# Kernel tuning notes

Hardware: AMD Instinct MI355X
Metric: run time of the kernel (lower is better)

## Reference

```python
import jax, jax.numpy as jnp
import numpy as np

B, LQ, LK, DK, DV = 32, 128, 4096, 256, 256


def setup_inputs() -> dict:
    key = jax.random.key(0)
    k1, k2, k3, k4, k5 = jax.random.split(key, 5)
    return {
        "query": jax.random.normal(k1, (B, LQ, DK), dtype=jnp.float32),
        "query_lengths": jax.random.randint(k2, (B,), 1, LQ, dtype=jnp.int32),
        "keys": jax.random.normal(k3, (B, LK, DK), dtype=jnp.float32),
        "values": jax.random.normal(k4, (B, LK, DV), dtype=jnp.float32),
        "mask": jax.random.randint(k5, (B, LK), 0, 2, dtype=jnp.int32),  # 1 = masked out
    }


def reference(query, query_lengths, keys, values, mask):
    # zero query positions beyond each example's length (torch: mask_query masked_fill 0)
    q_valid = jnp.arange(query.shape[1])[None, :] < query_lengths[:, None]  # [B, Lq]
    query = jnp.where(q_valid[:, :, None], query, 0.0)
    # zero masked key/value timesteps (torch mask: 1 -> masked)
    kv_valid = (mask == 0)[:, :, None]  # [B, Lk, 1]
    keys = jnp.where(kv_valid, keys, 0.0)
    values = jnp.where(kv_valid, values, 0.0)
    # attention scores [B, Lq, Lk]
    weights = jnp.einsum("bqd,bkd->bqk", query, keys)
    # exact-zero scores (masked rows/cols) -> -inf, matching torch weights==0.0 fill
    weights = jnp.where(weights == 0.0, -jnp.inf, weights)
    weights = jax.nn.softmax(weights, axis=-1)
    # rows that were all -inf produce NaN -> cleaned to 0
    weights = jnp.where(jnp.isnan(weights), 0.0, weights)
    attended = jnp.einsum("bqk,bkv->bqv", weights, values)  # [B, Lq, Dv]
    return jnp.mean(attended, axis=1)  # [B, Dv]
```

## Files before the change

### kernel.cpp

```cpp
#include <hip/hip_runtime.h>
#include <hip/hip_fp16.h>
#include <stdint.h>

#define NB  32
#define NLQ 128
#define NLK 4096
#define NDK 256
#define NDV 256
#define KT  32
#define SPLITS 8

typedef _Float16 f16;
typedef _Float16 f16x4 __attribute__((ext_vector_type(4)));
typedef _Float16 f16x8 __attribute__((ext_vector_type(8)));
typedef float    f32x4 __attribute__((ext_vector_type(4)));

__global__ __launch_bounds__(512) void fvta_part1(
    const float* __restrict__ q_, const float* __restrict__ k_,
    const float* __restrict__ v_, const int* __restrict__ mask_,
    f16* __restrict__ accw, float* __restrict__ mlw)
{
    __shared__ __align__(16) f16 KA[2][KT * NDK];
    __shared__ __align__(16) int MK[NLK / SPLITS];

    const int tid = threadIdx.x, w = tid >> 6, lane = tid & 63;
    const int l15 = lane & 15, lhi = lane >> 4;
    const int s = blockIdx.x, b = blockIdx.y, S = gridDim.x;
    const int slice = NLK / S, nt = slice / KT, kbase = s * slice;
    const float NEG = -__builtin_inff();

    const float* kb = k_ + ((size_t)b * NLK + kbase) * NDK;
    const float* vb = v_ + ((size_t)b * NLK + kbase) * NDV;
    const int*   mb = mask_ + b * NLK + kbase;

    if (tid < slice) MK[tid] = mb[tid];

    f16x8 qf[8];
    {
        const float* qrow = q_ + ((size_t)b * NLQ + w * 16 + l15) * NDK + lhi * 8;
        #pragma unroll
        for (int kd = 0; kd < 8; ++kd) {
            f32x4 x = *(const f32x4*)(qrow + kd * 32);
            f32x4 y = *(const f32x4*)(qrow + kd * 32 + 4);
            f16x8 f;
            f[0]=(f16)x[0]; f[1]=(f16)x[1]; f[2]=(f16)x[2]; f[3]=(f16)x[3];
            f[4]=(f16)y[0]; f[5]=(f16)y[1]; f[6]=(f16)y[2]; f[7]=(f16)y[3];
            qf[kd] = f;
        }
    }

    f32x4 accu[16];
    #pragma unroll
    for (int i = 0; i < 16; ++i) accu[i] = (f32x4){0.f, 0.f, 0.f, 0.f};
    float m_run = NEG, l_run = 0.f;

    f32x4 ks[4];

    auto stage = [&](f16* KAb) {
        #pragma unroll
        for (int r = 0; r < 4; ++r) {
            const int kk = r * 8 + w;
            const int d  = lane * 4;
            const int e  = kk * NDK + (d ^ ((kk & 15) << 3));
            f32x4 x = ks[r];
            f16x4 hh; hh[0]=(f16)x[0]; hh[1]=(f16)x[1]; hh[2]=(f16)x[2]; hh[3]=(f16)x[3];
            *(f16x4*)(KAb + e) = hh;
        }
    };

    #pragma unroll
    for (int r = 0; r < 4; ++r)
        ks[r] = *(const f32x4*)(kb + (r * 512 + tid) * 4);
    stage(KA[0]);
    __syncthreads();

    const int swz = l15 << 3;

    for (int t = 0; t < nt; ++t) {
        const int cur = t & 1;
        if (t + 1 < nt) {
            const float* ksrc = kb + (size_t)(t + 1) * KT * NDK;
            #pragma unroll
            for (int r = 0; r < 4; ++r)
                ks[r] = *(const f32x4*)(ksrc + (r * 512 + tid) * 4);
        }
        const int k0 = t * KT;

        f32x4 s4a = (f32x4){0.f,0.f,0.f,0.f}, s4b = s4a;
        {
            const f16* k0p = &KA[cur][(0 * 16 + l15) * NDK];
            const f16* k1p = &KA[cur][(1 * 16 + l15) * NDK];
            #pragma unroll
            for (int kd = 0; kd < 8; ++kd) {
                const int col = (kd * 32 + lhi * 8) ^ swz;
                f16x8 kfa = *(const f16x8*)(k0p + col);
                s4a = __builtin_amdgcn_mfma_f32_16x16x32_f16(kfa, qf[kd], s4a, 0, 0, 0);
                f16x8 kfb = *(const f16x8*)(k1p + col);
                s4b = __builtin_amdgcn_mfma_f32_16x16x32_f16(kfb, qf[kd], s4b, 0, 0, 0);
            }
        }

        const int4 m4a = *(const int4*)(MK + k0 + lhi * 4);
        const int4 m4b = *(const int4*)(MK + k0 + 16 + lhi * 4);
        float sa[4], sb[4];
        sa[0] = m4a.x ? NEG : s4a[0]; sa[1] = m4a.y ? NEG : s4a[1];
        sa[2] = m4a.z ? NEG : s4a[2]; sa[3] = m4a.w ? NEG : s4a[3];
        sb[0] = m4b.x ? NEG : s4b[0]; sb[1] = m4b.y ? NEG : s4b[1];
        sb[2] = m4b.z ? NEG : s4b[2]; sb[3] = m4b.w ? NEG : s4b[3];

        float tmax = fmaxf(fmaxf(fmaxf(sa[0], sa[1]), fmaxf(sa[2], sa[3])),
                           fmaxf(fmaxf(sb[0], sb[1]), fmaxf(sb[2], sb[3])));
        tmax = fmaxf(tmax, __shfl_xor(tmax, 16, 64));
        tmax = fmaxf(tmax, __shfl_xor(tmax, 32, 64));
        const float mnew = fmaxf(m_run, tmax);
        const bool  dead = (mnew == NEG);
        const float scale = dead ? 1.f : __expf(m_run - mnew);
        float pa4[4], pb4[4];
        #pragma unroll
        for (int j = 0; j < 4; ++j) {
            pa4[j] = dead ? 0.f : __expf(sa[j] - mnew);
            pb4[j] = dead ? 0.f : __expf(sb[j] - mnew);
        }
        float ps = (pa4[0] + pa4[1]) + (pa4[2] + pa4[3])
                 + (pb4[0] + pb4[1]) + (pb4[2] + pb4[3]);
        ps += __shfl_xor(ps, 16, 64);
        ps += __shfl_xor(ps, 32, 64);
        l_run = l_run * scale + ps;
        m_run = mnew;

        f16x4 pa, pb;
        pa[0]=(f16)pa4[0]; pa[1]=(f16)pa4[1]; pa[2]=(f16)pa4[2]; pa[3]=(f16)pa4[3];
        pb[0]=(f16)pb4[0]; pb[1]=(f16)pb4[1]; pb[2]=(f16)pb4[2]; pb[3]=(f16)pb4[3];

        if (!__all(scale == 1.f)) {
            float scj[4];
            #pragma unroll
            for (int j = 0; j < 4; ++j) scj[j] = __shfl(scale, lhi * 4 + j, 64);
            #pragma unroll
            for (int d = 0; d < 16; ++d) {
                accu[d][0] *= scj[0]; accu[d][1] *= scj[1];
                accu[d][2] *= scj[2]; accu[d][3] *= scj[3];
            }
        }

        {
            const float* vr = vb + (size_t)(k0 + lhi * 4) * NDV + l15;
            #pragma unroll
            for (int h = 0; h < 2; ++h) {
                const f16x4 pfrag = h ? pb : pa;
                const float* vh = vr + (size_t)h * 16 * NDV;
                #pragma unroll
                for (int dg = 0; dg < 4; ++dg) {
                    float tv[4][4];
                    #pragma unroll
                    for (int dd = 0; dd < 4; ++dd) {
                        const float* vc = vh + (dg * 4 + dd) * 16;
                        tv[dd][0] = vc[0];
                        tv[dd][1] = vc[1 * NDV];
                        tv[dd][2] = vc[2 * NDV];
                        tv[dd][3] = vc[3 * NDV];
                    }
                    #pragma unroll
                    for (int dd = 0; dd < 4; ++dd) {
                        f16x4 vf;
                        vf[0]=(f16)tv[dd][0]; vf[1]=(f16)tv[dd][1];
                        vf[2]=(f16)tv[dd][2]; vf[3]=(f16)tv[dd][3];
                        accu[dg * 4 + dd] = __builtin_amdgcn_mfma_f32_16x16x16f16(
                            pfrag, vf, accu[dg * 4 + dd], 0, 0, 0);
                    }
                }
            }
        }

        if (t + 1 < nt) stage(KA[cur ^ 1]);
        __syncthreads();
    }

    const size_t base = (size_t)(b * S + s) * NLQ + w * 16;
    #pragma unroll
    for (int j = 0; j < 4; ++j) {
        f16* dst = accw + (base + lhi * 4 + j) * NDV + l15;
        #pragma unroll
        for (int d = 0; d < 16; ++d) dst[d * 16] = (f16)accu[d][j];
    }
    if (lane < 16) {
        mlw[(base + lane) * 2]     = m_run;
        mlw[(base + lane) * 2 + 1] = l_run;
    }
}

__global__ __launch_bounds__(256) void fvta_merge(
    const f16* __restrict__ accw, const float* __restrict__ mlw,
    const int* __restrict__ qlen_, float* __restrict__ out_, int S)
{
    __shared__ float fac[16][SPLITS + 1];
    const int qc = blockIdx.x, b = blockIdx.y, tid = threadIdx.x;
    const int len = qlen_[b];
    const float NEG = -__builtin_inff();

    if (tid < 16) {
        const int q = qc * 16 + tid;
        if (q < len) {
            float gm = NEG;
            for (int ss = 0; ss < S; ++ss)
                gm = fmaxf(gm, mlw[((size_t)(b * S + ss) * NLQ + q) * 2]);
            float L = 0.f;
            for (int ss = 0; ss < S; ++ss) {
                const float m = mlw[((size_t)(b * S + ss) * NLQ + q) * 2];
                const float l = mlw[((size_t)(b * S + ss) * NLQ + q) * 2 + 1];
                if (m != NEG) L += l * __expf(m - gm);
            }
            for (int ss = 0; ss < S; ++ss) {
                const float m = mlw[((size_t)(b * S + ss) * NLQ + q) * 2];
                fac[tid][ss] = (gm != NEG && L > 0.f && m != NEG)
                             ? __expf(m - gm) / L : 0.f;
            }
        } else {
            for (int ss = 0; ss < S; ++ss) fac[tid][ss] = 0.f;
        }
    }
    __syncthreads();

    float sum = 0.f;
    for (int qq = 0; qq < 16; ++qq) {
        const int q = qc * 16 + qq;
        for (int ss = 0; ss < S; ++ss) {
            const float f = fac[qq][ss];
            if (f != 0.f)
                sum += (float)accw[((size_t)(b * S + ss) * NLQ + q) * NDV + tid] * f;
        }
    }
    atomicAdd(&out_[b * NDV + tid], sum * (1.f / NLQ));
}

extern "C" void kernel_launch(void* const* d_in, const int* in_sizes, int n_in,
                              void* d_out, int out_size, void* d_ws, size_t ws_size,
                              hipStream_t stream) {
    const float* q    = (const float*)d_in[0];
    const int*   qlen = (const int*)d_in[1];
    const float* k    = (const float*)d_in[2];
    const float* v    = (const float*)d_in[3];
    const int*   mask = (const int*)d_in[4];
    float* out = (float*)d_out;

    int S = SPLITS;
    while (S > 1 && ((size_t)NB * S * NLQ * NDV * 2 + (size_t)NB * S * NLQ * 8) > ws_size)
        S >>= 1;
    f16*   accw = (f16*)d_ws;
    float* mlw  = (float*)((char*)d_ws + (size_t)NB * S * NLQ * NDV * 2);

    hipMemsetAsync(out, 0, (size_t)out_size * sizeof(float), stream);
    dim3 g1(S, NB);
    fvta_part1<<<g1, 512, 0, stream>>>(q, k, v, mask, accw, mlw);
    dim3 g2(NLQ / 16, NB);
    fvta_merge<<<g2, 256, 0, stream>>>(accw, mlw, qlen, out, S);
}
```

Measured before the change: 139.8 us.

## Load K directly from global memory instead of staging through LDS

Removes the double-buffered shared-memory staging of K tiles and the per-tile barrier; each wave now loads its K fragments from global memory and converts them to fp16 in registers. This is meant to cut LDS traffic and synchronisation. The cost is that all eight waves re-read the same K rows, which multiplies global/L2 traffic and exposes load latency without prefetch. It also halves the query rows per merge block and drops the workspace-size fallback for the split count, which assumes the workspace is always large enough.

```diff
diff --git a/kernel.cpp b/kernel.cpp
--- a/kernel.cpp
+++ b/kernel.cpp
@@ -20,8 +20,7 @@
     const float* __restrict__ v_, const int* __restrict__ mask_,
     f16* __restrict__ accw, float* __restrict__ mlw)
 {
-    __shared__ __align__(16) f16 KA[2][KT * NDK];
-    __shared__ __align__(16) int MK[NLK / SPLITS];
+    __shared__ int MK[NLK / SPLITS];
 
     const int tid = threadIdx.x, w = tid >> 6, lane = tid & 63;
     const int l15 = lane & 15, lhi = lane >> 4;
@@ -33,7 +32,7 @@
     const float* vb = v_ + ((size_t)b * NLK + kbase) * NDV;
     const int*   mb = mask_ + b * NLK + kbase;
 
-    if (tid < slice) MK[tid] = mb[tid];
+    for (int i = tid; i < slice; i += 512) MK[i] = mb[i];
 
     f16x8 qf[8];
     {
@@ -54,48 +53,27 @@
     for (int i = 0; i < 16; ++i) accu[i] = (f32x4){0.f, 0.f, 0.f, 0.f};
     float m_run = NEG, l_run = 0.f;
 
-    f32x4 ks[4];
-
-    auto stage = [&](f16* KAb) {
-        #pragma unroll
-        for (int r = 0; r < 4; ++r) {
-            const int kk = r * 8 + w;
-            const int d  = lane * 4;
-            const int e  = kk * NDK + (d ^ ((kk & 15) << 3));
-            f32x4 x = ks[r];
-            f16x4 hh; hh[0]=(f16)x[0]; hh[1]=(f16)x[1]; hh[2]=(f16)x[2]; hh[3]=(f16)x[3];
-            *(f16x4*)(KAb + e) = hh;
-        }
-    };
-
-    #pragma unroll
-    for (int r = 0; r < 4; ++r)
-        ks[r] = *(const f32x4*)(kb + (r * 512 + tid) * 4);
-    stage(KA[0]);
     __syncthreads();
 
-    const int swz = l15 << 3;
-
     for (int t = 0; t < nt; ++t) {
-        const int cur = t & 1;
-        if (t + 1 < nt) {
-            const float* ksrc = kb + (size_t)(t + 1) * KT * NDK;
-            #pragma unroll
-            for (int r = 0; r < 4; ++r)
-                ks[r] = *(const f32x4*)(ksrc + (r * 512 + tid) * 4);
-        }
         const int k0 = t * KT;
 
         f32x4 s4a = (f32x4){0.f,0.f,0.f,0.f}, s4b = s4a;
         {
-            const f16* k0p = &KA[cur][(0 * 16 + l15) * NDK];
-            const f16* k1p = &KA[cur][(1 * 16 + l15) * NDK];
+            const float* ka_row = kb + (size_t)(k0 + l15) * NDK + lhi * 8;
+            const float* kb_row = ka_row + 16 * NDK;
             #pragma unroll
             for (int kd = 0; kd < 8; ++kd) {
-                const int col = (kd * 32 + lhi * 8) ^ swz;
-                f16x8 kfa = *(const f16x8*)(k0p + col);
+                f32x4 xa = *(const f32x4*)(ka_row + kd * 32);
+                f32x4 ya = *(const f32x4*)(ka_row + kd * 32 + 4);
+                f32x4 xb = *(const f32x4*)(kb_row + kd * 32);
+                f32x4 yb = *(const f32x4*)(kb_row + kd * 32 + 4);
+                f16x8 kfa, kfb;
+                kfa[0]=(f16)xa[0]; kfa[1]=(f16)xa[1]; kfa[2]=(f16)xa[2]; kfa[3]=(f16)xa[3];
+                kfa[4]=(f16)ya[0]; kfa[5]=(f16)ya[1]; kfa[6]=(f16)ya[2]; kfa[7]=(f16)ya[3];
+                kfb[0]=(f16)xb[0]; kfb[1]=(f16)xb[1]; kfb[2]=(f16)xb[2]; kfb[3]=(f16)xb[3];
+                kfb[4]=(f16)yb[0]; kfb[5]=(f16)yb[1]; kfb[6]=(f16)yb[2]; kfb[7]=(f16)yb[3];
                 s4a = __builtin_amdgcn_mfma_f32_16x16x32_f16(kfa, qf[kd], s4a, 0, 0, 0);
-                f16x8 kfb = *(const f16x8*)(k1p + col);
                 s4b = __builtin_amdgcn_mfma_f32_16x16x32_f16(kfb, qf[kd], s4b, 0, 0, 0);
             }
         }
@@ -171,9 +149,6 @@
                 }
             }
         }
-
-        if (t + 1 < nt) stage(KA[cur ^ 1]);
-        __syncthreads();
     }
 
     const size_t base = (size_t)(b * S + s) * NLQ + w * 16;
@@ -193,13 +168,13 @@
     const f16* __restrict__ accw, const float* __restrict__ mlw,
     const int* __restrict__ qlen_, float* __restrict__ out_, int S)
 {
-    __shared__ float fac[16][SPLITS + 1];
+    __shared__ float fac[8][SPLITS + 1];
     const int qc = blockIdx.x, b = blockIdx.y, tid = threadIdx.x;
     const int len = qlen_[b];
     const float NEG = -__builtin_inff();
 
-    if (tid < 16) {
-        const int q = qc * 16 + tid;
+    if (tid < 8) {
+        const int q = qc * 8 + tid;
         if (q < len) {
             float gm = NEG;
             for (int ss = 0; ss < S; ++ss)
@@ -222,8 +197,8 @@
     __syncthreads();
 
     float sum = 0.f;
-    for (int qq = 0; qq < 16; ++qq) {
-        const int q = qc * 16 + qq;
+    for (int qq = 0; qq < 8; ++qq) {
+        const int q = qc * 8 + qq;
         for (int ss = 0; ss < S; ++ss) {
             const float f = fac[qq][ss];
             if (f != 0.f)
@@ -243,15 +218,13 @@
     const int*   mask = (const int*)d_in[4];
     float* out = (float*)d_out;
 
-    int S = SPLITS;
-    while (S > 1 && ((size_t)NB * S * NLQ * NDV * 2 + (size_t)NB * S * NLQ * 8) > ws_size)
-        S >>= 1;
+    const int S = SPLITS;
     f16*   accw = (f16*)d_ws;
     float* mlw  = (float*)((char*)d_ws + (size_t)NB * S * NLQ * NDV * 2);
 
     hipMemsetAsync(out, 0, (size_t)out_size * sizeof(float), stream);
     dim3 g1(S, NB);
     fvta_part1<<<g1, 512, 0, stream>>>(q, k, v, mask, accw, mlw);
-    dim3 g2(NLQ / 16, NB);
+    dim3 g2(NLQ / 8, NB);
     fvta_merge<<<g2, 256, 0, stream>>>(accw, mlw, qlen, out, S);
 }
```

Result: slower. 214.3 us (+53.3%).
